# Optimization experiments

Hardware: AMD Instinct MI355X
Metric: run time of the kernel (lower is better)

## Reference

```python
import jax, jax.numpy as jnp
import numpy as np

B, NB, PL, FD, H = 32, 64, 20, 4096, 1024


def setup_inputs() -> dict:
    key = jax.random.key(0)
    k1, k2, k3, k4, k5 = jax.random.split(key, 5)
    vision = jax.random.normal(k1, (B, NB, FD), dtype=jnp.float32)
    language = jax.random.normal(k2, (B, NB, PL, H), dtype=jnp.float32)
    phrase_lengths = jax.random.randint(k3, (B, NB), 1, PL + 1, dtype=jnp.int32)
    # Xavier-uniform initialized Linear params, zero bias (as in module)
    lim_v = float(np.sqrt(6.0 / (FD + H)))
    lim_l = float(np.sqrt(6.0 / (H + H)))
    Wv = jax.random.uniform(k4, (FD, H), minval=-lim_v, maxval=lim_v, dtype=jnp.float32)
    bv = jnp.zeros((H,), dtype=jnp.float32)
    Wl = jax.random.uniform(k5, (H, H), minval=-lim_l, maxval=lim_l, dtype=jnp.float32)
    bl = jnp.zeros((H,), dtype=jnp.float32)
    return {"vision": vision, "language": language, "phrase_lengths": phrase_lengths,
            "Wv": Wv, "bv": bv, "Wl": Wl, "bl": bl}


def reference(vision, language, phrase_lengths, Wv, bv, Wl, bl):
    # Vectorized replacement of the per-region loop: sum over phrase tokens,
    # divide by the (data-dependent) phrase length.  [B, NB, H]
    pooled = jnp.sum(language, axis=2) / phrase_lengths[..., None].astype(language.dtype)
    # Multimodal branch: both mappings applied.
    visual_map = jnp.einsum('bnf,fh->bnh', vision, Wv) + bv    # [B, NB, H]
    language_map = jnp.einsum('bnh,hk->bnk', pooled, Wl) + bl  # [B, NB, H]
    return (language_map, visual_map)
```

## Files before the change

kernel.cpp:

```cpp
#include <hip/hip_runtime.h>
#include <hip/hip_bf16.h>
#include <stdint.h>

#define B_   32
#define NB_  64
#define PL_  20
#define FD_  4096
#define H_   1024
#define M_   (B_ * NB_)

typedef short bf16x8 __attribute__((ext_vector_type(8)));
typedef float f32x4  __attribute__((ext_vector_type(4)));

__device__ __forceinline__ ushort f2bf(float f) {
    uint32_t u = __builtin_bit_cast(uint32_t, f);
    u += 0x7fffu + ((u >> 16) & 1u);
    return (ushort)(u >> 16);
}

__global__ __launch_bounds__(256) void prep_kernel(
    const float* __restrict__ lang, const int* __restrict__ plen,
    ushort* __restrict__ pooled,
    const float* __restrict__ vision, ushort* __restrict__ visionb,
    const float* __restrict__ Wv, ushort* __restrict__ WvT,
    const float* __restrict__ Wl, ushort* __restrict__ WlT)
{
    __shared__ float tile[32][33];
    int blk = blockIdx.x;
    int tid = threadIdx.x;

    if (blk < M_) {
        int r = blk;
        int h = tid << 2;
        const float* base = lang + (size_t)r * (PL_ * H_) + h;
        float sx = 0.f, sy = 0.f, sz = 0.f, sw = 0.f;
#pragma unroll
        for (int p = 0; p < PL_; ++p) {
            float4 v = *(const float4*)(base + (size_t)p * H_);
            sx += v.x; sy += v.y; sz += v.z; sw += v.w;
        }
        float inv = 1.0f / (float)plen[r];
        ushort4 o = make_ushort4(f2bf(sx * inv), f2bf(sy * inv),
                                 f2bf(sz * inv), f2bf(sw * inv));
        *(ushort4*)(pooled + (size_t)r * H_ + h) = o;
    } else if (blk < M_ + 8192) {
        int i = (blk - M_) * 256 + tid;
        float4 v = ((const float4*)vision)[i];
        ushort4 o = make_ushort4(f2bf(v.x), f2bf(v.y), f2bf(v.z), f2bf(v.w));
        ((ushort4*)visionb)[i] = o;
    } else {
        const float* W; ushort* Wt; int K, b;
        if (blk < M_ + 8192 + 4096) { W = Wv; Wt = WvT; K = FD_; b = blk - (M_ + 8192); }
        else                        { W = Wl; Wt = WlT; K = H_;  b = blk - (M_ + 8192 + 4096); }
        int n0 = (b & 31) * 32, k0 = (b >> 5) * 32;
        int tx = tid & 31, ty = tid >> 5;
#pragma unroll
        for (int i = 0; i < 32; i += 8)
            tile[ty + i][tx] = W[(size_t)(k0 + ty + i) * H_ + n0 + tx];
        __syncthreads();
#pragma unroll
        for (int i = 0; i < 32; i += 8)
            Wt[(size_t)(n0 + ty + i) * K + k0 + tx] = f2bf(tile[tx][ty + i]);
    }
}

#define BM 128
#define BN 128
#define BK 64

__device__ __forceinline__ void async16(const void* g, void* l) {
    __builtin_amdgcn_global_load_lds(
        (const __attribute__((address_space(1))) void*)g,
        (__attribute__((address_space(3))) void*)l, 16, 0, 0);
}

__device__ __forceinline__ void stage_tile(
    const char* Ag, const char* Bg, size_t Kb, size_t ko,
    char* AsB, char* BsB, int tid)
{
#pragma unroll
    for (int j = 0; j < 4; ++j) {
        int off = j * 4096 + tid * 16;
        int row = off >> 7;
        int cbl = off & 127;
        int cbg = cbl ^ ((row & 7) << 4);
        async16(Ag + (size_t)row * Kb + ko + cbg, AsB + off);
        async16(Bg + (size_t)row * Kb + ko + cbg, BsB + off);
    }
}

__global__ __launch_bounds__(256) void gemm_bt_dual(
    const ushort* __restrict__ A1, const ushort* __restrict__ Bt1,
    const float* __restrict__ bias1, float* __restrict__ C1,
    const ushort* __restrict__ A2, const ushort* __restrict__ Bt2,
    const float* __restrict__ bias2, float* __restrict__ C2)
{
    __shared__ ushort As[2][BM * BK];
    __shared__ ushort Bs[2][BN * BK];

    int wg = blockIdx.x;
    bool isV = wg < 384;
    int w, ks, nk, k0s;
    if (isV) {
        ks = wg >> 7;
        w  = wg & 127;
        nk  = (ks == 0) ? 22 : 21;
        k0s = (ks == 0) ? 0 : (22 + (ks - 1) * 21);
    } else {
        ks = 0; w = wg - 384; nk = 16; k0s = 0;
    }
    int y = w & 7, x = w >> 3;

    const ushort* A   = isV ? A1 : A2;
    const ushort* Bt  = isV ? Bt1 : Bt2;
    const float* bias = isV ? bias1 : bias2;
    float* C          = isV ? C1 : C2;
    int K             = isV ? FD_ : H_;

    const int N = H_;
    int tid  = threadIdx.x;
    int wave = tid >> 6, lane = tid & 63;
    int lx = lane & 15, lz = lane >> 4;
    int wr = wave >> 1, wc = wave & 1;
    int row0 = x * BM;
    int col0 = y * BN;

    size_t Kb = (size_t)K * 2;

    const char* Ag = (const char*)A  + (size_t)row0 * Kb;
    const char* Bg = (const char*)Bt + (size_t)col0 * Kb;

    int sw = (lx & 7) << 4;

    f32x4 acc[4][4] = {};

    stage_tile(Ag, Bg, Kb, (size_t)k0s * 128,       (char*)As[0], (char*)Bs[0], tid);
    stage_tile(Ag, Bg, Kb, (size_t)(k0s + 1) * 128, (char*)As[1], (char*)Bs[1], tid);

    for (int kt = 0; kt < nk; ++kt) {
        if (kt < nk - 1) asm volatile("s_waitcnt vmcnt(8)" ::: "memory");
        else             asm volatile("s_waitcnt vmcnt(0)" ::: "memory");
        __builtin_amdgcn_s_barrier();

        const char* Ab = (const char*)As[kt & 1];
        const char* Bb = (const char*)Bs[kt & 1];
        bf16x8 af[2][4], bfr[2][4];
#pragma unroll
        for (int kk = 0; kk < 2; ++kk) {
#pragma unroll
            for (int m = 0; m < 4; ++m)
                af[kk][m] = *(const bf16x8*)(Ab +
                    (wr * 64 + m * 16 + lx) * 128 + ((kk * 64 + lz * 16) ^ sw));
#pragma unroll
            for (int n = 0; n < 4; ++n)
                bfr[kk][n] = *(const bf16x8*)(Bb +
                    (wc * 64 + n * 16 + lx) * 128 + ((kk * 64 + lz * 16) ^ sw));
        }
        asm volatile("s_waitcnt lgkmcnt(0)" ::: "memory");
        __builtin_amdgcn_s_barrier();

        if (kt + 2 < nk)
            stage_tile(Ag, Bg, Kb, (size_t)(k0s + kt + 2) * 128,
                       (char*)As[kt & 1], (char*)Bs[kt & 1], tid);

#pragma unroll
        for (int kk = 0; kk < 2; ++kk)
#pragma unroll
            for (int m = 0; m < 4; ++m)
#pragma unroll
                for (int n = 0; n < 4; ++n)
                    acc[m][n] = __builtin_amdgcn_mfma_f32_16x16x32_bf16(
                        af[kk][m], bfr[kk][n], acc[m][n], 0, 0, 0);
    }

#pragma unroll
    for (int m = 0; m < 4; ++m) {
        int row = row0 + wr * 64 + m * 16 + lz * 4;
#pragma unroll
        for (int n = 0; n < 4; ++n) {
            int col = col0 + wc * 64 + n * 16 + lx;
            float bb = (ks == 0) ? bias[col] : 0.f;
            if (isV) {
#pragma unroll
                for (int r = 0; r < 4; ++r)
                    atomicAdd(&C[(size_t)(row + r) * N + col],
                              acc[m][n][r] + bb);
            } else {
#pragma unroll
                for (int r = 0; r < 4; ++r)
                    C[(size_t)(row + r) * N + col] = acc[m][n][r] + bb;
            }
        }
    }
}

extern "C" void kernel_launch(void* const* d_in, const int* in_sizes, int n_in,
                              void* d_out, int out_size, void* d_ws, size_t ws_size,
                              hipStream_t stream) {
    const float* vision   = (const float*)d_in[0];
    const float* language = (const float*)d_in[1];
    const int*   plen     = (const int*)d_in[2];
    const float* Wv       = (const float*)d_in[3];
    const float* bv       = (const float*)d_in[4];
    const float* Wl       = (const float*)d_in[5];
    const float* bl       = (const float*)d_in[6];

    float* out      = (float*)d_out;
    float* lang_map = out;
    float* vis_map  = out + (size_t)M_ * H_;

    char* ws = (char*)d_ws;
    ushort* pooled  = (ushort*)(ws);
    ushort* visionb = (ushort*)(ws + (4u  << 20));
    ushort* WvT     = (ushort*)(ws + (20u << 20));
    ushort* WlT     = (ushort*)(ws + (28u << 20));

    hipMemsetAsync(vis_map, 0, (size_t)M_ * H_ * sizeof(float), stream);

    hipLaunchKernelGGL(prep_kernel, dim3(15360), dim3(256), 0, stream,
                       language, plen, pooled, vision, visionb,
                       Wv, WvT, Wl, WlT);
    hipLaunchKernelGGL(gemm_bt_dual, dim3(512), dim3(256), 0, stream,
                       visionb, WvT, bv, vis_map,
                       pooled,  WlT, bl, lang_map);
}
```

Measured before the change: 91.43 us.

## Switch GEMM to BK=32 triple-buffered LDS pipeline with single barrier per step

Halves the K tile to 32 and moves from two LDS buffers to three, so the next-next tile is issued right after the barrier and the second barrier per iteration is removed. Iteration counts and the split-K boundaries for the vision GEMM are recomputed for the smaller tile, and the XOR swizzle is adapted to 64-byte rows. The aim is to overlap global-to-LDS loads with MFMA work and cut synchronisation stalls. In exchange there are twice as many loop iterations, each with less MFMA work to hide latency behind, and the swizzle may be less effective at avoiding LDS bank conflicts.

```diff
diff --git a/kernel.cpp b/kernel.cpp
--- a/kernel.cpp
+++ b/kernel.cpp
@@ -66,7 +66,7 @@
 
 #define BM 128
 #define BN 128
-#define BK 64
+#define BK 32
 
 __device__ __forceinline__ void async16(const void* g, void* l) {
     __builtin_amdgcn_global_load_lds(
@@ -79,11 +79,11 @@
     char* AsB, char* BsB, int tid)
 {
 #pragma unroll
-    for (int j = 0; j < 4; ++j) {
+    for (int j = 0; j < 2; ++j) {
         int off = j * 4096 + tid * 16;
-        int row = off >> 7;
-        int cbl = off & 127;
-        int cbg = cbl ^ ((row & 7) << 4);
+        int row = off >> 6;
+        int cbl = off & 63;
+        int cbg = cbl ^ ((row & 3) << 4);
         async16(Ag + (size_t)row * Kb + ko + cbg, AsB + off);
         async16(Bg + (size_t)row * Kb + ko + cbg, BsB + off);
     }
@@ -95,8 +95,8 @@
     const ushort* __restrict__ A2, const ushort* __restrict__ Bt2,
     const float* __restrict__ bias2, float* __restrict__ C2)
 {
-    __shared__ ushort As[2][BM * BK];
-    __shared__ ushort Bs[2][BN * BK];
+    __shared__ ushort As[3][BM * BK];
+    __shared__ ushort Bs[3][BN * BK];
 
     int wg = blockIdx.x;
     bool isV = wg < 384;
@@ -104,10 +104,10 @@
     if (isV) {
         ks = wg >> 7;
         w  = wg & 127;
-        nk  = (ks == 0) ? 22 : 21;
-        k0s = (ks == 0) ? 0 : (22 + (ks - 1) * 21);
+        nk  = (ks == 2) ? 42 : 43;
+        k0s = ks * 43;
     } else {
-        ks = 0; w = wg - 384; nk = 16; k0s = 0;
+        ks = 0; w = wg - 384; nk = 32; k0s = 0;
     }
     int y = w & 7, x = w >> 3;
 
@@ -130,47 +130,43 @@
     const char* Ag = (const char*)A  + (size_t)row0 * Kb;
     const char* Bg = (const char*)Bt + (size_t)col0 * Kb;
 
-    int sw = (lx & 7) << 4;
+    int sw = (lx & 3) << 4;
 
     f32x4 acc[4][4] = {};
 
-    stage_tile(Ag, Bg, Kb, (size_t)k0s * 128,       (char*)As[0], (char*)Bs[0], tid);
-    stage_tile(Ag, Bg, Kb, (size_t)(k0s + 1) * 128, (char*)As[1], (char*)Bs[1], tid);
-
+    stage_tile(Ag, Bg, Kb, (size_t)k0s * 64,       (char*)As[0], (char*)Bs[0], tid);
+    stage_tile(Ag, Bg, Kb, (size_t)(k0s + 1) * 64, (char*)As[1], (char*)Bs[1], tid);
+
+    int cur = 0;
     for (int kt = 0; kt < nk; ++kt) {
-        if (kt < nk - 1) asm volatile("s_waitcnt vmcnt(8)" ::: "memory");
+        if (kt < nk - 1) asm volatile("s_waitcnt vmcnt(4)" ::: "memory");
         else             asm volatile("s_waitcnt vmcnt(0)" ::: "memory");
         __builtin_amdgcn_s_barrier();
 
-        const char* Ab = (const char*)As[kt & 1];
-        const char* Bb = (const char*)Bs[kt & 1];
-        bf16x8 af[2][4], bfr[2][4];
-#pragma unroll
-        for (int kk = 0; kk < 2; ++kk) {
-#pragma unroll
-            for (int m = 0; m < 4; ++m)
-                af[kk][m] = *(const bf16x8*)(Ab +
-                    (wr * 64 + m * 16 + lx) * 128 + ((kk * 64 + lz * 16) ^ sw));
+        int stg = cur + 2; if (stg >= 3) stg -= 3;
+        if (kt + 2 < nk)
+            stage_tile(Ag, Bg, Kb, (size_t)(k0s + kt + 2) * 64,
+                       (char*)As[stg], (char*)Bs[stg], tid);
+
+        const char* Ab = (const char*)As[cur];
+        const char* Bb = (const char*)Bs[cur];
+        bf16x8 af[4], bfr[4];
+#pragma unroll
+        for (int m = 0; m < 4; ++m)
+            af[m] = *(const bf16x8*)(Ab +
+                (wr * 64 + m * 16 + lx) * 64 + ((lz * 16) ^ sw));
+#pragma unroll
+        for (int n = 0; n < 4; ++n)
+            bfr[n] = *(const bf16x8*)(Bb +
+                (wc * 64 + n * 16 + lx) * 64 + ((lz * 16) ^ sw));
+#pragma unroll
+        for (int m = 0; m < 4; ++m)
 #pragma unroll
             for (int n = 0; n < 4; ++n)
-                bfr[kk][n] = *(const bf16x8*)(Bb +
-                    (wc * 64 + n * 16 + lx) * 128 + ((kk * 64 + lz * 16) ^ sw));
-        }
-        asm volatile("s_waitcnt lgkmcnt(0)" ::: "memory");
-        __builtin_amdgcn_s_barrier();
-
-        if (kt + 2 < nk)
-            stage_tile(Ag, Bg, Kb, (size_t)(k0s + kt + 2) * 128,
-                       (char*)As[kt & 1], (char*)Bs[kt & 1], tid);
-
-#pragma unroll
-        for (int kk = 0; kk < 2; ++kk)
-#pragma unroll
-            for (int m = 0; m < 4; ++m)
-#pragma unroll
-                for (int n = 0; n < 4; ++n)
-                    acc[m][n] = __builtin_amdgcn_mfma_f32_16x16x32_bf16(
-                        af[kk][m], bfr[kk][n], acc[m][n], 0, 0, 0);
+                acc[m][n] = __builtin_amdgcn_mfma_f32_16x16x32_bf16(
+                    af[m], bfr[n], acc[m][n], 0, 0, 0);
+
+        cur = (cur + 1 == 3) ? 0 : cur + 1;
     }
 
 #pragma unroll
```

After: 101.4 us. 10.9% more time.

## Overlap language pooling with vision GEMM and split-K the language GEMM

Applied to the files above, without the earlier changes.

Moves the memory-bound language pooling (reading the large language tensor) out of the prep kernel and into extra blocks of the vision GEMM launch, so the pooling's bandwidth-heavy reads can run alongside the compute-bound vision GEMM. The language GEMM becomes its own launch with split-K over two slices using atomic adds, which requires zeroing both outputs in the memset. This adds a kernel launch and doubles the memset size, and the pooling blocks compete with GEMM tiles for CUs.

```diff
diff --git a/kernel.cpp b/kernel.cpp
--- a/kernel.cpp
+++ b/kernel.cpp
@@ -18,19 +18,155 @@
     return (ushort)(u >> 16);
 }
 
-__global__ __launch_bounds__(256) void prep_kernel(
-    const float* __restrict__ lang, const int* __restrict__ plen,
-    ushort* __restrict__ pooled,
+__global__ __launch_bounds__(256) void prep_small(
     const float* __restrict__ vision, ushort* __restrict__ visionb,
     const float* __restrict__ Wv, ushort* __restrict__ WvT,
     const float* __restrict__ Wl, ushort* __restrict__ WlT)
 {
     __shared__ float tile[32][33];
-    int blk = blockIdx.x;
-    int tid = threadIdx.x;
-
-    if (blk < M_) {
-        int r = blk;
+    int blk = blockIdx.x, tid = threadIdx.x;
+    if (blk < 8192) {
+        int i = blk * 256 + tid;
+        float4 v = ((const float4*)vision)[i];
+        ushort4 o = make_ushort4(f2bf(v.x), f2bf(v.y), f2bf(v.z), f2bf(v.w));
+        ((ushort4*)visionb)[i] = o;
+    } else {
+        const float* W; ushort* Wt; int K, b;
+        if (blk < 12288) { W = Wv; Wt = WvT; K = FD_; b = blk - 8192; }
+        else             { W = Wl; Wt = WlT; K = H_;  b = blk - 12288; }
+        int n0 = (b & 31) * 32, k0 = (b >> 5) * 32;
+        int tx = tid & 31, ty = tid >> 5;
+#pragma unroll
+        for (int i = 0; i < 32; i += 8)
+            tile[ty + i][tx] = W[(size_t)(k0 + ty + i) * H_ + n0 + tx];
+        __syncthreads();
+#pragma unroll
+        for (int i = 0; i < 32; i += 8)
+            Wt[(size_t)(n0 + ty + i) * K + k0 + tx] = f2bf(tile[tx][ty + i]);
+    }
+}
+
+#define BM 128
+#define BN 128
+#define BK 64
+
+__device__ __forceinline__ void async16(const void* g, void* l) {
+    __builtin_amdgcn_global_load_lds(
+        (const __attribute__((address_space(1))) void*)g,
+        (__attribute__((address_space(3))) void*)l, 16, 0, 0);
+}
+
+__device__ __forceinline__ void stage_tile(
+    const char* Ag, const char* Bg, size_t Kb, size_t ko,
+    char* AsB, char* BsB, int tid)
+{
+#pragma unroll
+    for (int j = 0; j < 4; ++j) {
+        int off = j * 4096 + tid * 16;
+        int row = off >> 7;
+        int cbl = off & 127;
+        int cbg = cbl ^ ((row & 7) << 4);
+        async16(Ag + (size_t)row * Kb + ko + cbg, AsB + off);
+        async16(Bg + (size_t)row * Kb + ko + cbg, BsB + off);
+    }
+}
+
+__device__ __forceinline__ void gemm_bt_core(
+    const char* Ag, const char* Bg, size_t Kb, int k0s, int nk,
+    ushort (*As)[BM * BK], ushort (*Bs)[BN * BK],
+    int tid, int wr, int wc, int lx, int lz, f32x4 acc[4][4])
+{
+    int sw = (lx & 7) << 4;
+
+    stage_tile(Ag, Bg, Kb, (size_t)k0s * 128,       (char*)As[0], (char*)Bs[0], tid);
+    stage_tile(Ag, Bg, Kb, (size_t)(k0s + 1) * 128, (char*)As[1], (char*)Bs[1], tid);
+
+    for (int kt = 0; kt < nk; ++kt) {
+        if (kt < nk - 1) asm volatile("s_waitcnt vmcnt(8)" ::: "memory");
+        else             asm volatile("s_waitcnt vmcnt(0)" ::: "memory");
+        __builtin_amdgcn_s_barrier();
+
+        const char* Ab = (const char*)As[kt & 1];
+        const char* Bb = (const char*)Bs[kt & 1];
+        bf16x8 af[2][4], bfr[2][4];
+#pragma unroll
+        for (int kk = 0; kk < 2; ++kk) {
+#pragma unroll
+            for (int m = 0; m < 4; ++m)
+                af[kk][m] = *(const bf16x8*)(Ab +
+                    (wr * 64 + m * 16 + lx) * 128 + ((kk * 64 + lz * 16) ^ sw));
+#pragma unroll
+            for (int n = 0; n < 4; ++n)
+                bfr[kk][n] = *(const bf16x8*)(Bb +
+                    (wc * 64 + n * 16 + lx) * 128 + ((kk * 64 + lz * 16) ^ sw));
+        }
+        asm volatile("s_waitcnt lgkmcnt(0)" ::: "memory");
+        __builtin_amdgcn_s_barrier();
+
+        if (kt + 2 < nk)
+            stage_tile(Ag, Bg, Kb, (size_t)(k0s + kt + 2) * 128,
+                       (char*)As[kt & 1], (char*)Bs[kt & 1], tid);
+
+#pragma unroll
+        for (int kk = 0; kk < 2; ++kk)
+#pragma unroll
+            for (int m = 0; m < 4; ++m)
+#pragma unroll
+                for (int n = 0; n < 4; ++n)
+                    acc[m][n] = __builtin_amdgcn_mfma_f32_16x16x32_bf16(
+                        af[kk][m], bfr[kk][n], acc[m][n], 0, 0, 0);
+    }
+}
+
+__device__ __forceinline__ void gemm_epilogue(
+    float* C, const float* bias, int ks, int row0, int col0,
+    int wr, int wc, int lx, int lz, f32x4 acc[4][4])
+{
+#pragma unroll
+    for (int m = 0; m < 4; ++m) {
+        int row = row0 + wr * 64 + m * 16 + lz * 4;
+#pragma unroll
+        for (int n = 0; n < 4; ++n) {
+            int col = col0 + wc * 64 + n * 16 + lx;
+            float bb = (ks == 0) ? bias[col] : 0.f;
+#pragma unroll
+            for (int r = 0; r < 4; ++r)
+                atomicAdd(&C[(size_t)(row + r) * H_ + col],
+                          acc[m][n][r] + bb);
+        }
+    }
+}
+
+__global__ __launch_bounds__(256) void gemm_vision_pool(
+    const ushort* __restrict__ Av, const ushort* __restrict__ Btv,
+    const float* __restrict__ bv, float* __restrict__ Cv,
+    const float* __restrict__ lang, const int* __restrict__ plen,
+    ushort* __restrict__ pooled)
+{
+    __shared__ ushort As[2][BM * BK];
+    __shared__ ushort Bs[2][BN * BK];
+
+    int wg = blockIdx.x, tid = threadIdx.x;
+    if (wg < 384) {
+        int ks = wg >> 7;
+        int w  = wg & 127;
+        int nk  = (ks == 0) ? 22 : 21;
+        int k0s = (ks == 0) ? 0 : (22 + (ks - 1) * 21);
+        int y = w & 7, x = w >> 3;
+
+        int wave = tid >> 6, lane = tid & 63;
+        int lx = lane & 15, lz = lane >> 4;
+        int wr = wave >> 1, wc = wave & 1;
+
+        size_t Kb = (size_t)FD_ * 2;
+        const char* Ag = (const char*)Av  + (size_t)(x * BM) * Kb;
+        const char* Bg = (const char*)Btv + (size_t)(y * BN) * Kb;
+
+        f32x4 acc[4][4] = {};
+        gemm_bt_core(Ag, Bg, Kb, k0s, nk, As, Bs, tid, wr, wc, lx, lz, acc);
+        gemm_epilogue(Cv, bv, ks, x * BM, y * BN, wr, wc, lx, lz, acc);
+    } else {
+        int r = wg - 384;
         int h = tid << 2;
         const float* base = lang + (size_t)r * (PL_ * H_) + h;
         float sx = 0.f, sy = 0.f, sz = 0.f, sw = 0.f;
@@ -43,155 +179,33 @@
         ushort4 o = make_ushort4(f2bf(sx * inv), f2bf(sy * inv),
                                  f2bf(sz * inv), f2bf(sw * inv));
         *(ushort4*)(pooled + (size_t)r * H_ + h) = o;
-    } else if (blk < M_ + 8192) {
-        int i = (blk - M_) * 256 + tid;
-        float4 v = ((const float4*)vision)[i];
-        ushort4 o = make_ushort4(f2bf(v.x), f2bf(v.y), f2bf(v.z), f2bf(v.w));
-        ((ushort4*)visionb)[i] = o;
-    } else {
-        const float* W; ushort* Wt; int K, b;
-        if (blk < M_ + 8192 + 4096) { W = Wv; Wt = WvT; K = FD_; b = blk - (M_ + 8192); }
-        else                        { W = Wl; Wt = WlT; K = H_;  b = blk - (M_ + 8192 + 4096); }
-        int n0 = (b & 31) * 32, k0 = (b >> 5) * 32;
-        int tx = tid & 31, ty = tid >> 5;
-#pragma unroll
-        for (int i = 0; i < 32; i += 8)
-            tile[ty + i][tx] = W[(size_t)(k0 + ty + i) * H_ + n0 + tx];
-        __syncthreads();
-#pragma unroll
-        for (int i = 0; i < 32; i += 8)
-            Wt[(size_t)(n0 + ty + i) * K + k0 + tx] = f2bf(tile[tx][ty + i]);
-    }
-}
-
-#define BM 128
-#define BN 128
-#define BK 64
-
-__device__ __forceinline__ void async16(const void* g, void* l) {
-    __builtin_amdgcn_global_load_lds(
-        (const __attribute__((address_space(1))) void*)g,
-        (__attribute__((address_space(3))) void*)l, 16, 0, 0);
-}
-
-__device__ __forceinline__ void stage_tile(
-    const char* Ag, const char* Bg, size_t Kb, size_t ko,
-    char* AsB, char* BsB, int tid)
-{
-#pragma unroll
-    for (int j = 0; j < 4; ++j) {
-        int off = j * 4096 + tid * 16;
-        int row = off >> 7;
-        int cbl = off & 127;
-        int cbg = cbl ^ ((row & 7) << 4);
-        async16(Ag + (size_t)row * Kb + ko + cbg, AsB + off);
-        async16(Bg + (size_t)row * Kb + ko + cbg, BsB + off);
-    }
-}
-
-__global__ __launch_bounds__(256) void gemm_bt_dual(
-    const ushort* __restrict__ A1, const ushort* __restrict__ Bt1,
-    const float* __restrict__ bias1, float* __restrict__ C1,
-    const ushort* __restrict__ A2, const ushort* __restrict__ Bt2,
-    const float* __restrict__ bias2, float* __restrict__ C2)
+    }
+}
+
+__global__ __launch_bounds__(256) void gemm_lang(
+    const ushort* __restrict__ Al, const ushort* __restrict__ Btl,
+    const float* __restrict__ bl, float* __restrict__ Cl)
 {
     __shared__ ushort As[2][BM * BK];
     __shared__ ushort Bs[2][BN * BK];
 
-    int wg = blockIdx.x;
-    bool isV = wg < 384;
-    int w, ks, nk, k0s;
-    if (isV) {
-        ks = wg >> 7;
-        w  = wg & 127;
-        nk  = (ks == 0) ? 22 : 21;
-        k0s = (ks == 0) ? 0 : (22 + (ks - 1) * 21);
-    } else {
-        ks = 0; w = wg - 384; nk = 16; k0s = 0;
-    }
+    int wg = blockIdx.x, tid = threadIdx.x;
+    int ks = wg >> 7;
+    int w  = wg & 127;
+    int nk = 8, k0s = ks * 8;
     int y = w & 7, x = w >> 3;
 
-    const ushort* A   = isV ? A1 : A2;
-    const ushort* Bt  = isV ? Bt1 : Bt2;
-    const float* bias = isV ? bias1 : bias2;
-    float* C          = isV ? C1 : C2;
-    int K             = isV ? FD_ : H_;
-
-    const int N = H_;
-    int tid  = threadIdx.x;
     int wave = tid >> 6, lane = tid & 63;
     int lx = lane & 15, lz = lane >> 4;
     int wr = wave >> 1, wc = wave & 1;
-    int row0 = x * BM;
-    int col0 = y * BN;
-
-    size_t Kb = (size_t)K * 2;
-
-    const char* Ag = (const char*)A  + (size_t)row0 * Kb;
-    const char* Bg = (const char*)Bt + (size_t)col0 * Kb;
-
-    int sw = (lx & 7) << 4;
+
+    size_t Kb = (size_t)H_ * 2;
+    const char* Ag = (const char*)Al  + (size_t)(x * BM) * Kb;
+    const char* Bg = (const char*)Btl + (size_t)(y * BN) * Kb;
 
     f32x4 acc[4][4] = {};
-
-    stage_tile(Ag, Bg, Kb, (size_t)k0s * 128,       (char*)As[0], (char*)Bs[0], tid);
-    stage_tile(Ag, Bg, Kb, (size_t)(k0s + 1) * 128, (char*)As[1], (char*)Bs[1], tid);
-
-    for (int kt = 0; kt < nk; ++kt) {
-        if (kt < nk - 1) asm volatile("s_waitcnt vmcnt(8)" ::: "memory");
-        else             asm volatile("s_waitcnt vmcnt(0)" ::: "memory");
-        __builtin_amdgcn_s_barrier();
-
-        const char* Ab = (const char*)As[kt & 1];
-        const char* Bb = (const char*)Bs[kt & 1];
-        bf16x8 af[2][4], bfr[2][4];
-#pragma unroll
-        for (int kk = 0; kk < 2; ++kk) {
-#pragma unroll
-            for (int m = 0; m < 4; ++m)
-                af[kk][m] = *(const bf16x8*)(Ab +
-                    (wr * 64 + m * 16 + lx) * 128 + ((kk * 64 + lz * 16) ^ sw));
-#pragma unroll
-            for (int n = 0; n < 4; ++n)
-                bfr[kk][n] = *(const bf16x8*)(Bb +
-                    (wc * 64 + n * 16 + lx) * 128 + ((kk * 64 + lz * 16) ^ sw));
-        }
-        asm volatile("s_waitcnt lgkmcnt(0)" ::: "memory");
-        __builtin_amdgcn_s_barrier();
-
-        if (kt + 2 < nk)
-            stage_tile(Ag, Bg, Kb, (size_t)(k0s + kt + 2) * 128,
-                       (char*)As[kt & 1], (char*)Bs[kt & 1], tid);
-
-#pragma unroll
-        for (int kk = 0; kk < 2; ++kk)
-#pragma unroll
-            for (int m = 0; m < 4; ++m)
-#pragma unroll
-                for (int n = 0; n < 4; ++n)
-                    acc[m][n] = __builtin_amdgcn_mfma_f32_16x16x32_bf16(
-                        af[kk][m], bfr[kk][n], acc[m][n], 0, 0, 0);
-    }
-
-#pragma unroll
-    for (int m = 0; m < 4; ++m) {
-        int row = row0 + wr * 64 + m * 16 + lz * 4;
-#pragma unroll
-        for (int n = 0; n < 4; ++n) {
-            int col = col0 + wc * 64 + n * 16 + lx;
-            float bb = (ks == 0) ? bias[col] : 0.f;
-            if (isV) {
-#pragma unroll
-                for (int r = 0; r < 4; ++r)
-                    atomicAdd(&C[(size_t)(row + r) * N + col],
-                              acc[m][n][r] + bb);
-            } else {
-#pragma unroll
-                for (int r = 0; r < 4; ++r)
-                    C[(size_t)(row + r) * N + col] = acc[m][n][r] + bb;
-            }
-        }
-    }
+    gemm_bt_core(Ag, Bg, Kb, k0s, nk, As, Bs, tid, wr, wc, lx, lz, acc);
+    gemm_epilogue(Cl, bl, ks, x * BM, y * BN, wr, wc, lx, lz, acc);
 }
 
 extern "C" void kernel_launch(void* const* d_in, const int* in_sizes, int n_in,
@@ -215,12 +229,13 @@
     ushort* WvT     = (ushort*)(ws + (20u << 20));
     ushort* WlT     = (ushort*)(ws + (28u << 20));
 
-    hipMemsetAsync(vis_map, 0, (size_t)M_ * H_ * sizeof(float), stream);
-
-    hipLaunchKernelGGL(prep_kernel, dim3(15360), dim3(256), 0, stream,
-                       language, plen, pooled, vision, visionb,
-                       Wv, WvT, Wl, WlT);
-    hipLaunchKernelGGL(gemm_bt_dual, dim3(512), dim3(256), 0, stream,
+    hipMemsetAsync(out, 0, (size_t)2 * M_ * H_ * sizeof(float), stream);
+
+    hipLaunchKernelGGL(prep_small, dim3(13312), dim3(256), 0, stream,
+                       vision, visionb, Wv, WvT, Wl, WlT);
+    hipLaunchKernelGGL(gemm_vision_pool, dim3(2432), dim3(256), 0, stream,
                        visionb, WvT, bv, vis_map,
-                       pooled,  WlT, bl, lang_map);
-}
+                       language, plen, pooled);
+    hipLaunchKernelGGL(gemm_lang, dim3(256), dim3(256), 0, stream,
+                       pooled, WlT, bl, lang_map);
+}
```

New measurement: 100.6 us. 10.0% more time.
